# Kernel tuning notes

Measured on AMD Instinct MI355X. Metric: run time of the kernel, lower is better.

Reference implementation:

```python
import jax, jax.numpy as jnp
import numpy as np

EPS = 1e-05


def setup_inputs() -> dict:
    key = jax.random.key(0)
    ks = jax.random.split(key, 6)
    B, L, D = 16, 4096, 1024
    x = jax.random.normal(ks[0], (B, L, D), dtype=jnp.float32)
    prev_count = jax.random.randint(ks[1], (B,), 1, 5).astype(jnp.int32)  # prior_count-like, >=1
    prev_mean = jnp.zeros((B, D), dtype=jnp.float32)   # prior_mean init = 0
    prev_var = jnp.ones((B, D), dtype=jnp.float32)     # exp(prior_logv) with logv init 0
    weight = 0.02 * jax.random.normal(ks[2], (D,), dtype=jnp.float32)
    bias = 0.02 * jax.random.normal(ks[3], (D,), dtype=jnp.float32)
    padding_mask = jax.random.randint(ks[4], (B, L), 0, 2).astype(bool)  # True = padded
    return {"x": x, "prev_count": prev_count, "prev_mean": prev_mean,
            "prev_var": prev_var, "weight": weight, "bias": bias,
            "padding_mask": padding_mask}


def _timestep_norm(x, prev_count, prev_mean, prev_var, gamma, beta, padding_mask, eps):
    # x: [B, L, D]; Welford running mean/var over timesteps, skipping padded steps.
    B, L, D = x.shape
    valid = (~padding_mask).astype(x.dtype)          # [B, L], 1 = valid step
    x_t = jnp.swapaxes(x, 0, 1)                      # [L, B, D]
    m_t = valid.T                                    # [L, B]

    def step(carry, inp):
        count, mean, var = carry                     # [B], [B,D], [B,D]
        xt, m = inp                                  # [B,D], [B]
        mb = m[:, None]                              # [B,1]
        new_count = count + m                        # [B]
        denom = jnp.maximum(new_count, 1.0)[:, None]
        delta = xt - mean
        new_mean = mean + mb * delta / denom
        var_upd = (count[:, None] * var + delta * (xt - new_mean)) / denom
        new_var = jnp.where(mb > 0, var_upd, var)
        y = (gamma * (xt - new_mean) * jax.lax.rsqrt(new_var + eps) + beta) * mb
        return (new_count, new_mean, new_var), y

    init = (prev_count.astype(x.dtype), prev_mean, prev_var)
    (count, mean, var), ys = jax.lax.scan(step, init, (x_t, m_t))
    y = jnp.swapaxes(ys, 0, 1)                       # [B, L, D]
    return y, count, mean, var


def reference(x, prev_count, prev_mean, prev_var, weight, bias, padding_mask):
    gamma = weight + 1.0
    return _timestep_norm(x, prev_count, prev_mean, prev_var, gamma, bias,
                          padding_mask, EPS)
```

## Files before the change

kernel.cpp:

```cpp
#include <hip/hip_runtime.h>


#define Bn 16
#define Ln 4096
#define Dn 1024
#define D4 (Dn / 4)
#define Cn 128
#define CLn (Ln / Cn)
#define NCH (Bn * Cn)
#define SEG 32
#define EPSf 1e-5f

struct St { float n; float4 m; float4 s; };

__device__ __forceinline__ St chan_merge(const St& A, const St& B) {
    St R;
    R.n = A.n + B.n;
    float wB = B.n / fmaxf(R.n, 1.f);
    float sc = A.n * wB;
    float dx = B.m.x - A.m.x, dy = B.m.y - A.m.y,
          dz = B.m.z - A.m.z, dw = B.m.w - A.m.w;
    R.m.x = A.m.x + dx * wB; R.m.y = A.m.y + dy * wB;
    R.m.z = A.m.z + dz * wB; R.m.w = A.m.w + dw * wB;
    R.s.x = A.s.x + B.s.x + dx * dx * sc; R.s.y = A.s.y + B.s.y + dy * dy * sc;
    R.s.z = A.s.z + B.s.z + dz * dz * sc; R.s.w = A.s.w + B.s.w + dw * dw * sc;
    return R;
}

__global__ __launch_bounds__(256) void tn_chunk_stats(
    const float* __restrict__ x, const int* __restrict__ mask,
    float4* __restrict__ agg_mean, float4* __restrict__ agg_m2,
    float* __restrict__ agg_n)
{
    int bc = blockIdx.x;
    int d4 = threadIdx.x;
    const float4* xp = (const float4*)(x + (size_t)bc * CLn * Dn) + d4;
    const int4*   mp = (const int4*)(mask + bc * CLn);

    int4 mrow[CLn / 4];
    #pragma unroll
    for (int i = 0; i < CLn / 4; ++i) mrow[i] = mp[i];
    const int* mr = (const int*)mrow;

    St A; A.n = 0.f; A.m = {0.f, 0.f, 0.f, 0.f}; A.s = {0.f, 0.f, 0.f, 0.f};
    #pragma unroll 8
    for (int i = 0; i < CLn; ++i) {
        if (mr[i] == 0) {
            float4 xv = xp[(size_t)i * D4];
            A.n += 1.f;
            float rn = 1.f / A.n;
            float dx;
            dx = xv.x - A.m.x; A.m.x += dx * rn; A.s.x += dx * (xv.x - A.m.x);
            dx = xv.y - A.m.y; A.m.y += dx * rn; A.s.y += dx * (xv.y - A.m.y);
            dx = xv.z - A.m.z; A.m.z += dx * rn; A.s.z += dx * (xv.z - A.m.z);
            dx = xv.w - A.m.w; A.m.w += dx * rn; A.s.w += dx * (xv.w - A.m.w);
        }
    }
    agg_mean[(size_t)bc * D4 + d4] = A.m;
    agg_m2  [(size_t)bc * D4 + d4] = A.s;
    if (d4 == 0) agg_n[bc] = A.n;
}

__global__ __launch_bounds__(256) void tn_scan(
    const int* __restrict__ prev_count, const float4* __restrict__ prev_mean,
    const float4* __restrict__ prev_var,
    const float4* __restrict__ agg_mean, const float4* __restrict__ agg_m2,
    const float* __restrict__ agg_n,
    float4* __restrict__ pref_mean, float4* __restrict__ pref_m2,
    float* __restrict__ pref_n,
    float* __restrict__ out_count, float4* __restrict__ out_mean,
    float4* __restrict__ out_var)
{
    __shared__ St lds[4][64];
    int g   = blockIdx.x & 3;
    int b   = blockIdx.x >> 2;
    int d4l = threadIdx.x & 63;
    int q   = threadIdx.x >> 6;
    int d4  = g * 64 + d4l;
    int c0  = q * SEG;

    St S; S.n = 0.f; S.m = {0.f, 0.f, 0.f, 0.f}; S.s = {0.f, 0.f, 0.f, 0.f};
    #pragma unroll 4
    for (int i = 0; i < SEG; ++i) {
        int ch = b * Cn + c0 + i;
        St ag;
        ag.n = agg_n[ch];
        ag.m = agg_mean[(size_t)ch * D4 + d4];
        ag.s = agg_m2  [(size_t)ch * D4 + d4];
        S = chan_merge(S, ag);
    }
    lds[q][d4l] = S;
    __syncthreads();

    St E;
    E.n = (float)prev_count[b];
    E.m = prev_mean[b * D4 + d4];
    float4 vp = prev_var[b * D4 + d4];
    E.s = {vp.x * E.n, vp.y * E.n, vp.z * E.n, vp.w * E.n};
    #pragma unroll
    for (int j = 0; j < 3; ++j)
        if (j < q) E = chan_merge(E, lds[j][d4l]);

    #pragma unroll 4
    for (int i = 0; i < SEG; ++i) {
        int ch = b * Cn + c0 + i;
        pref_mean[(size_t)ch * D4 + d4] = E.m;
        pref_m2  [(size_t)ch * D4 + d4] = E.s;
        if (d4 == 0) pref_n[ch] = E.n;
        St ag;
        ag.n = agg_n[ch];
        ag.m = agg_mean[(size_t)ch * D4 + d4];
        ag.s = agg_m2  [(size_t)ch * D4 + d4];
        E = chan_merge(E, ag);
    }

    if (q == 3) {
        out_mean[b * D4 + d4] = E.m;
        float rn = 1.f / E.n;
        out_var[b * D4 + d4] = {E.s.x * rn, E.s.y * rn, E.s.z * rn, E.s.w * rn};
        if (d4 == 0) out_count[b] = E.n;
    }
}

__global__ __launch_bounds__(256) void tn_emit(
    const float* __restrict__ x, const int* __restrict__ mask,
    const float* __restrict__ weight, const float* __restrict__ bias,
    const float4* __restrict__ pref_mean, const float4* __restrict__ pref_m2,
    const float* __restrict__ pref_n, float* __restrict__ y)
{
    int bc = blockIdx.x;
    int d4 = threadIdx.x;
    size_t gbase = (size_t)bc * CLn * Dn;
    const float4* xp = (const float4*)(x + gbase) + d4;
    float4*       yp = (float4*)(y + gbase) + d4;
    const int4*   mp = (const int4*)(mask + bc * CLn);

    int4 mrow[CLn / 4];
    #pragma unroll
    for (int i = 0; i < CLn / 4; ++i) mrow[i] = mp[i];
    const int* mr = (const int*)mrow;

    float  n    = pref_n[bc];
    float4 mean = pref_mean[(size_t)bc * D4 + d4];
    float4 M2   = pref_m2  [(size_t)bc * D4 + d4];
    const float4 w4 = ((const float4*)weight)[d4];
    const float4 b4 = ((const float4*)bias)[d4];
    float gx = w4.x + 1.f, gy = w4.y + 1.f, gz = w4.z + 1.f, gw = w4.w + 1.f;

    #pragma unroll 4
    for (int i = 0; i < CLn; ++i) {
        float4 yv = {0.f, 0.f, 0.f, 0.f};
        if (mr[i] == 0) {
            float4 xv = xp[(size_t)i * D4];
            n += 1.f;
            float rn = 1.f / n;
            float dx, d2;
            dx = xv.x - mean.x; mean.x += dx * rn; d2 = xv.x - mean.x;
            M2.x += dx * d2; yv.x = gx * d2 * rsqrtf(M2.x * rn + EPSf) + b4.x;
            dx = xv.y - mean.y; mean.y += dx * rn; d2 = xv.y - mean.y;
            M2.y += dx * d2; yv.y = gy * d2 * rsqrtf(M2.y * rn + EPSf) + b4.y;
            dx = xv.z - mean.z; mean.z += dx * rn; d2 = xv.z - mean.z;
            M2.z += dx * d2; yv.z = gz * d2 * rsqrtf(M2.z * rn + EPSf) + b4.z;
            dx = xv.w - mean.w; mean.w += dx * rn; d2 = xv.w - mean.w;
            M2.w += dx * d2; yv.w = gw * d2 * rsqrtf(M2.w * rn + EPSf) + b4.w;
        }
        yp[(size_t)i * D4] = yv;
    }
}

extern "C" void kernel_launch(void* const* d_in, const int* in_sizes, int n_in,
                              void* d_out, int out_size, void* d_ws, size_t ws_size,
                              hipStream_t stream)
{
    const float* x          = (const float*)d_in[0];
    const int*   prev_count = (const int*)d_in[1];
    const float* prev_mean  = (const float*)d_in[2];
    const float* prev_var   = (const float*)d_in[3];
    const float* weight     = (const float*)d_in[4];
    const float* bias       = (const float*)d_in[5];
    const int*   mask       = (const int*)d_in[6];

    float* y         = (float*)d_out;
    float* out_count = y + (size_t)Bn * Ln * Dn;
    float* out_mean  = out_count + Bn;
    float* out_var   = out_mean + (size_t)Bn * Dn;

    float4* agg_mean  = (float4*)d_ws;
    float4* agg_m2    = agg_mean  + (size_t)NCH * D4;
    float4* pref_mean = agg_m2    + (size_t)NCH * D4;
    float4* pref_m2   = pref_mean + (size_t)NCH * D4;
    float*  agg_n     = (float*)(pref_m2 + (size_t)NCH * D4);
    float*  pref_n    = agg_n + NCH;

    tn_chunk_stats<<<NCH, 256, 0, stream>>>(x, mask, agg_mean, agg_m2, agg_n);
    tn_scan<<<64, 256, 0, stream>>>(
        prev_count, (const float4*)prev_mean, (const float4*)prev_var,
        agg_mean, agg_m2, agg_n, pref_mean, pref_m2, pref_n,
        out_count, (float4*)out_mean, (float4*)out_var);
    tn_emit<<<NCH, 256, 0, stream>>>(
        x, mask, weight, bias, pref_mean, pref_m2, pref_n, y);
}
```

Measured before the change: 537.8 us.

## Parallelize chunk prefix scan with wavefront shuffles and use nontemporal output stores

The middle scan kernel is rewritten so that each 64-lane wavefront handles one (batch, d4) column. Each lane merges two chunks, then a Hillis-Steele shuffle-up scan combines the 128 chunk statistics, replacing the old 64-block serial loop over 32 chunks per quarter. This raises parallelism from 64 blocks to 1024 blocks, at the cost of strided global loads across channels. Separately, the emit kernel now writes y with nontemporal stores to avoid polluting cache with streaming output.

```diff
diff --git a/kernel.cpp b/kernel.cpp
--- a/kernel.cpp
+++ b/kernel.cpp
@@ -8,8 +8,9 @@
 #define Cn 128
 #define CLn (Ln / Cn)
 #define NCH (Bn * Cn)
-#define SEG 32
 #define EPSf 1e-5f
+
+typedef float f32x4 __attribute__((ext_vector_type(4)));
 
 struct St { float n; float4 m; float4 s; };
 
@@ -25,6 +26,16 @@
     R.s.x = A.s.x + B.s.x + dx * dx * sc; R.s.y = A.s.y + B.s.y + dy * dy * sc;
     R.s.z = A.s.z + B.s.z + dz * dz * sc; R.s.w = A.s.w + B.s.w + dw * dw * sc;
     return R;
+}
+
+__device__ __forceinline__ St shfl_up_st(const St& v, int delta) {
+    St r;
+    r.n   = __shfl_up(v.n,   delta, 64);
+    r.m.x = __shfl_up(v.m.x, delta, 64); r.m.y = __shfl_up(v.m.y, delta, 64);
+    r.m.z = __shfl_up(v.m.z, delta, 64); r.m.w = __shfl_up(v.m.w, delta, 64);
+    r.s.x = __shfl_up(v.s.x, delta, 64); r.s.y = __shfl_up(v.s.y, delta, 64);
+    r.s.z = __shfl_up(v.s.z, delta, 64); r.s.w = __shfl_up(v.s.w, delta, 64);
+    return r;
 }
 
 __global__ __launch_bounds__(256) void tn_chunk_stats(
@@ -71,54 +82,53 @@
     float* __restrict__ out_count, float4* __restrict__ out_mean,
     float4* __restrict__ out_var)
 {
-    __shared__ St lds[4][64];
-    int g   = blockIdx.x & 3;
-    int b   = blockIdx.x >> 2;
-    int d4l = threadIdx.x & 63;
-    int q   = threadIdx.x >> 6;
-    int d4  = g * 64 + d4l;
-    int c0  = q * SEG;
-
-    St S; S.n = 0.f; S.m = {0.f, 0.f, 0.f, 0.f}; S.s = {0.f, 0.f, 0.f, 0.f};
-    #pragma unroll 4
-    for (int i = 0; i < SEG; ++i) {
-        int ch = b * Cn + c0 + i;
-        St ag;
-        ag.n = agg_n[ch];
-        ag.m = agg_mean[(size_t)ch * D4 + d4];
-        ag.s = agg_m2  [(size_t)ch * D4 + d4];
-        S = chan_merge(S, ag);
-    }
-    lds[q][d4l] = S;
-    __syncthreads();
-
-    St E;
-    E.n = (float)prev_count[b];
-    E.m = prev_mean[b * D4 + d4];
+    int wv   = (blockIdx.x * 256 + threadIdx.x) >> 6;
+    int lane = threadIdx.x & 63;
+    int b  = wv >> 8;
+    int d4 = wv & (D4 - 1);
+    int c0 = 2 * lane, c1 = 2 * lane + 1;
+    int ch0 = b * Cn + c0, ch1 = b * Cn + c1;
+
+    St s0, s1;
+    s0.n = agg_n[ch0]; s0.m = agg_mean[(size_t)ch0 * D4 + d4]; s0.s = agg_m2[(size_t)ch0 * D4 + d4];
+    s1.n = agg_n[ch1]; s1.m = agg_mean[(size_t)ch1 * D4 + d4]; s1.s = agg_m2[(size_t)ch1 * D4 + d4];
+
+    St incl = chan_merge(s0, s1);
+    #pragma unroll
+    for (int off = 1; off < 64; off <<= 1) {
+        St t = shfl_up_st(incl, off);
+        if (lane >= off) incl = chan_merge(t, incl);
+    }
+    St epp = shfl_up_st(incl, 1);
+    if (lane == 0) {
+        epp.n = 0.f;
+        epp.m = {0.f, 0.f, 0.f, 0.f};
+        epp.s = {0.f, 0.f, 0.f, 0.f};
+    }
+
+    float np = (float)prev_count[b];
+    St P;
+    P.n = np;
+    P.m = prev_mean[b * D4 + d4];
     float4 vp = prev_var[b * D4 + d4];
-    E.s = {vp.x * E.n, vp.y * E.n, vp.z * E.n, vp.w * E.n};
-    #pragma unroll
-    for (int j = 0; j < 3; ++j)
-        if (j < q) E = chan_merge(E, lds[j][d4l]);
-
-    #pragma unroll 4
-    for (int i = 0; i < SEG; ++i) {
-        int ch = b * Cn + c0 + i;
-        pref_mean[(size_t)ch * D4 + d4] = E.m;
-        pref_m2  [(size_t)ch * D4 + d4] = E.s;
-        if (d4 == 0) pref_n[ch] = E.n;
-        St ag;
-        ag.n = agg_n[ch];
-        ag.m = agg_mean[(size_t)ch * D4 + d4];
-        ag.s = agg_m2  [(size_t)ch * D4 + d4];
-        E = chan_merge(E, ag);
-    }
-
-    if (q == 3) {
-        out_mean[b * D4 + d4] = E.m;
-        float rn = 1.f / E.n;
-        out_var[b * D4 + d4] = {E.s.x * rn, E.s.y * rn, E.s.z * rn, E.s.w * rn};
-        if (d4 == 0) out_count[b] = E.n;
+    P.s = {vp.x * np, vp.y * np, vp.z * np, vp.w * np};
+
+    St pref0 = chan_merge(P, epp);
+    St pref1 = chan_merge(pref0, s0);
+
+    pref_mean[(size_t)ch0 * D4 + d4] = pref0.m; pref_m2[(size_t)ch0 * D4 + d4] = pref0.s;
+    pref_mean[(size_t)ch1 * D4 + d4] = pref1.m; pref_m2[(size_t)ch1 * D4 + d4] = pref1.s;
+    if (d4 == 0) {
+        pref_n[ch0] = pref0.n;
+        pref_n[ch1] = pref1.n;
+    }
+
+    if (lane == 63) {
+        St tot = chan_merge(P, incl);
+        out_mean[b * D4 + d4] = tot.m;
+        float rn = 1.f / tot.n;
+        out_var[b * D4 + d4] = {tot.s.x * rn, tot.s.y * rn, tot.s.z * rn, tot.s.w * rn};
+        if (d4 == 0) out_count[b] = tot.n;
     }
 }
 
@@ -132,7 +142,7 @@
     int d4 = threadIdx.x;
     size_t gbase = (size_t)bc * CLn * Dn;
     const float4* xp = (const float4*)(x + gbase) + d4;
-    float4*       yp = (float4*)(y + gbase) + d4;
+    f32x4*        yp = (f32x4*)(y + gbase) + d4;
     const int4*   mp = (const int4*)(mask + bc * CLn);
 
     int4 mrow[CLn / 4];
@@ -149,7 +159,7 @@
 
     #pragma unroll 4
     for (int i = 0; i < CLn; ++i) {
-        float4 yv = {0.f, 0.f, 0.f, 0.f};
+        f32x4 yv = {0.f, 0.f, 0.f, 0.f};
         if (mr[i] == 0) {
             float4 xv = xp[(size_t)i * D4];
             n += 1.f;
@@ -164,7 +174,7 @@
             dx = xv.w - mean.w; mean.w += dx * rn; d2 = xv.w - mean.w;
             M2.w += dx * d2; yv.w = gw * d2 * rsqrtf(M2.w * rn + EPSf) + b4.w;
         }
-        yp[(size_t)i * D4] = yv;
+        __builtin_nontemporal_store(yv, &yp[(size_t)i * D4]);
     }
 }
 
@@ -193,7 +203,7 @@
     float*  pref_n    = agg_n + NCH;
 
     tn_chunk_stats<<<NCH, 256, 0, stream>>>(x, mask, agg_mean, agg_m2, agg_n);
-    tn_scan<<<64, 256, 0, stream>>>(
+    tn_scan<<<(Bn * D4) / 4, 256, 0, stream>>>(
         prev_count, (const float4*)prev_mean, (const float4*)prev_var,
         agg_mean, agg_m2, agg_n, pref_mean, pref_m2, pref_n,
         out_count, (float4*)out_mean, (float4*)out_var);
```

New measurement: 502.1 us. 1.07x faster.
